# Kernel optimization log

Hardware: AMD Instinct MI355X
Metric: run time of the kernel (lower is better)

## Reference

```python
import jax, jax.numpy as jnp
import numpy as np

B, N, L, D = 128, 1024, 512, 64


def setup_inputs() -> dict:
    key = jax.random.key(0)
    k1, k2 = jax.random.split(key)
    text_outputs = jax.random.normal(k1, (B, N, D), dtype=jnp.float32)
    image_outputs = jax.random.normal(k2, (B, L, D), dtype=jnp.float32)
    rng = np.random.RandomState(0)
    ntok = rng.randint(N // 4, N + 1, size=B)
    nreg = rng.randint(L // 4, L + 1, size=B)
    text_mask = (np.arange(N)[None, :] < ntok[:, None]).astype(np.float32)
    image_mask = (np.arange(L)[None, :] < nreg[:, None]).astype(np.float32)
    # impostor indices (torch code samples these with np.random inside forward;
    # here they are fixed constants for determinism), guaranteed != own index
    I_imp = rng.randint(0, B, size=B)
    S_imp = rng.randint(0, B, size=B)
    ar = np.arange(B)
    I_imp = np.where(I_imp == ar, (I_imp + 1) % B, I_imp).astype(np.int32)
    S_imp = np.where(S_imp == ar, (S_imp + 1) % B, S_imp).astype(np.int32)
    return {
        "text_outputs": text_outputs,
        "image_outputs": image_outputs,
        "text_mask": jnp.asarray(text_mask),
        "image_mask": jnp.asarray(image_mask),
        "I_imp_idx": jnp.asarray(I_imp),
        "S_imp_idx": jnp.asarray(S_imp),
    }


def _mean_max_sim(T, I, tmask, imask):
    # T: (N, D) tokens, I: (L, D) regions; masks select the ragged valid prefix.
    M = jnp.einsum('nd,ld->nl', T, I)                       # matchmap (N, L)
    neg = jnp.finfo(M.dtype).min
    mx = jnp.max(jnp.where(imask[None, :] > 0, M, neg), axis=1)  # max over regions
    return jnp.sum(mx * tmask) / jnp.sum(tmask)             # mean over valid tokens


def reference(text_outputs, image_outputs, text_mask, image_mask, I_imp_idx, S_imp_idx, margin=1.0):
    sim = jax.vmap(_mean_max_sim)
    anchor = sim(text_outputs, image_outputs, text_mask, image_mask)            # (B,)
    Simpsim = sim(text_outputs[S_imp_idx], image_outputs, text_mask[S_imp_idx], image_mask)
    Iimpsim = sim(text_outputs, image_outputs[I_imp_idx], text_mask, image_mask[I_imp_idx])
    # scalar per-sample hinge: term added only when margin+imp-anchor > 0 == relu
    per_sample = jax.nn.relu(margin + Iimpsim - anchor) + jax.nn.relu(margin + Simpsim - anchor)
    loss = jnp.sum(per_sample) / text_outputs.shape[0]
    return loss[None]  # torch returns shape (1,)
```

## Files before the change

### kernel.cpp

```cpp
#include <hip/hip_runtime.h>
#include <hip/hip_bf16.h>

#define B 128
#define N 1024
#define L 512
#define D 64

typedef float f32x4 __attribute__((ext_vector_type(4)));
typedef short bf16x8 __attribute__((ext_vector_type(8)));

__device__ inline bf16x8 cvt8(float4 f0, float4 f1) {
    union { __hip_bfloat162 h2[4]; bf16x8 v; } u;
    u.h2[0] = __float22bfloat162_rn(make_float2(f0.x, f0.y));
    u.h2[1] = __float22bfloat162_rn(make_float2(f0.z, f0.w));
    u.h2[2] = __float22bfloat162_rn(make_float2(f1.x, f1.y));
    u.h2[3] = __float22bfloat162_rn(make_float2(f1.z, f1.w));
    return u.v;
}

#define WS_NEED_PRE (8192 + (size_t)B * L * D * 2)

__global__ __launch_bounds__(64) void cnts_kernel(
        const float* __restrict__ tmask, const float* __restrict__ imask,
        int* __restrict__ cnts) {
    int row = blockIdx.x;
    int lane = threadIdx.x;
    float s = 0.f;
    if (row < B) {
        const float* p = tmask + (size_t)row * N;
        for (int i = lane; i < N; i += 64) s += p[i];
    } else {
        const float* p = imask + (size_t)(row - B) * L;
        for (int i = lane; i < L; i += 64) s += p[i];
    }
    for (int off = 32; off > 0; off >>= 1) s += __shfl_down(s, off);
    if (lane == 0) cnts[row] = (int)(s + 0.5f);
}

__global__ __launch_bounds__(256) void prep_kernel(
        const float* __restrict__ I, unsigned short* __restrict__ Ibf) {
    int blk = blockIdx.x;
    int tid = threadIdx.x;
    const float* src = I + (size_t)blk * 64 * D;
    unsigned short* dst = Ibf + (size_t)blk * 4096;
#pragma unroll
    for (int j = 0; j < 2; ++j) {
        int si = tid + j * 256;
        int r = si >> 3, seg = si & 7;
        const float4* p = (const float4*)(src + (size_t)si * 8);
        bf16x8 v = cvt8(p[0], p[1]);
        int h = seg >> 2, qq = seg & 3;
        int ci = ((r >> 4) * 2 + h) * 64 + qq * 16 + (r & 15);
        *(bf16x8*)(dst + (size_t)ci * 8) = v;
    }
}

template <bool PRE>
__global__ __launch_bounds__(256, 6) void sim_kernel(
        const float* __restrict__ T, const float* __restrict__ I,
        const unsigned short* __restrict__ Ibf, const int* __restrict__ cnts,
        const int* __restrict__ Iimp, const int* __restrict__ Simp,
        float* __restrict__ partials) {
    int blk = blockIdx.x;
    int chunk = blk & 3;
    int bs = blk >> 2;
    int b = bs & (B - 1);
    int s = bs >> 7;
    int Tb = b, Ib = b;
    if (s == 1) Tb = Simp[b];
    else if (s == 2) Ib = Iimp[b];
    int ntok = cnts[Tb];
    int nreg = cnts[B + Ib];

    int tid = threadIdx.x;
    int tok0 = chunk * 256;
    if (tok0 >= ntok) {
        if (tid == 0) partials[blk] = 0.f;
        return;
    }

    int w = tid >> 6;
    int lane = tid & 63;
    int q = lane >> 4;
    int c = lane & 15;

    __shared__ unsigned short ldsI[2][64 * D];
    __shared__ float wsum[4];

    int wt0 = tok0 + w * 64;
    bf16x8 afrag[4][2];
#pragma unroll
    for (int tt = 0; tt < 4; ++tt) {
        const float* trow = T + ((size_t)Tb * N + wt0 + tt * 16 + c) * D;
#pragma unroll
        for (int h = 0; h < 2; ++h) {
            const float4* p = (const float4*)(trow + h * 32 + q * 8);
            afrag[tt][h] = cvt8(p[0], p[1]);
        }
    }

    float mx[4][4];
#pragma unroll
    for (int tt = 0; tt < 4; ++tt)
#pragma unroll
        for (int i = 0; i < 4; ++i) mx[tt][i] = -3.0e38f;

    int r_loc[2], db_loc[2];
#pragma unroll
    for (int j = 0; j < 2; ++j) {
        int ci = tid + j * 256;
        int g = ci >> 6, ln = ci & 63;
        r_loc[j] = (g >> 1) * 16 + (ln & 15);
        db_loc[j] = (g & 1) * 32 + (ln >> 4) * 8;
    }

    int nchunks = (nreg + 63) >> 6;
    const char* img = (const char*)(Ibf + (size_t)Ib * 8 * 4096);
    const float* Ibase = I + (size_t)Ib * L * D;
    uint4 pb0, pb1;
    float4 pf[4];

    auto issue = [&](int k) {
        if (PRE) {
            const char* srcb = img + (size_t)k * 8192;
            pb0 = *(const uint4*)(srcb + (size_t)tid * 16);
            pb1 = *(const uint4*)(srcb + (size_t)(tid + 256) * 16);
        } else {
            int rbase = k * 64;
#pragma unroll
            for (int j = 0; j < 2; ++j) {
                int r = rbase + r_loc[j];
                if (r < nreg) {
                    const float4* p = (const float4*)(Ibase + (size_t)r * D + db_loc[j]);
                    pf[2 * j] = p[0];
                    pf[2 * j + 1] = p[1];
                } else {
                    pf[2 * j] = make_float4(0.f, 0.f, 0.f, 0.f);
                    pf[2 * j + 1] = make_float4(0.f, 0.f, 0.f, 0.f);
                }
            }
        }
    };
    auto store = [&](int k) {
        char* bufb = (char*)&ldsI[k & 1][0];
        if (PRE) {
            *(uint4*)(bufb + (size_t)tid * 16) = pb0;
            *(uint4*)(bufb + (size_t)(tid + 256) * 16) = pb1;
        } else {
#pragma unroll
            for (int j = 0; j < 2; ++j) {
                int ci = tid + j * 256;
                *(bf16x8*)(bufb + (size_t)ci * 16) = cvt8(pf[2 * j], pf[2 * j + 1]);
            }
        }
    };

    issue(0);
    store(0);
    __syncthreads();

    for (int k = 0; k < nchunks; ++k) {
        if (k + 1 < nchunks) issue(k + 1);

        const char* base = (const char*)&ldsI[k & 1][0] + (size_t)lane * 16;
        int nvalid = nreg - k * 64;
        if (nvalid > 64) nvalid = 64;
        int nft = nvalid >> 4, prem = nvalid & 15;
        for (int rt = 0; rt < nft; ++rt) {
            bf16x8 b0 = *(const bf16x8*)(base + (size_t)(rt * 2 + 0) * 1024);
            bf16x8 b1 = *(const bf16x8*)(base + (size_t)(rt * 2 + 1) * 1024);
#pragma unroll
            for (int tt = 0; tt < 4; ++tt) {
                f32x4 acc = {0.f, 0.f, 0.f, 0.f};
                acc = __builtin_amdgcn_mfma_f32_16x16x32_bf16(afrag[tt][0], b0, acc, 0, 0, 0);
                acc = __builtin_amdgcn_mfma_f32_16x16x32_bf16(afrag[tt][1], b1, acc, 0, 0, 0);
#pragma unroll
                for (int i = 0; i < 4; ++i) mx[tt][i] = fmaxf(mx[tt][i], acc[i]);
            }
        }
        if (prem) {
            bf16x8 b0 = *(const bf16x8*)(base + (size_t)(nft * 2 + 0) * 1024);
            bf16x8 b1 = *(const bf16x8*)(base + (size_t)(nft * 2 + 1) * 1024);
            bool valid = c < prem;
#pragma unroll
            for (int tt = 0; tt < 4; ++tt) {
                f32x4 acc = {0.f, 0.f, 0.f, 0.f};
                acc = __builtin_amdgcn_mfma_f32_16x16x32_bf16(afrag[tt][0], b0, acc, 0, 0, 0);
                acc = __builtin_amdgcn_mfma_f32_16x16x32_bf16(afrag[tt][1], b1, acc, 0, 0, 0);
                if (valid) {
#pragma unroll
                    for (int i = 0; i < 4; ++i) mx[tt][i] = fmaxf(mx[tt][i], acc[i]);
                }
            }
        }

        if (k + 1 < nchunks) {
            store(k + 1);
            __syncthreads();
        }
    }

#pragma unroll
    for (int m = 1; m < 16; m <<= 1) {
#pragma unroll
        for (int tt = 0; tt < 4; ++tt)
#pragma unroll
            for (int i = 0; i < 4; ++i)
                mx[tt][i] = fmaxf(mx[tt][i], __shfl_xor(mx[tt][i], m));
    }

    float bsum = 0.f;
    if (c == 0) {
#pragma unroll
        for (int tt = 0; tt < 4; ++tt)
#pragma unroll
            for (int i = 0; i < 4; ++i) {
                int row = wt0 + tt * 16 + q * 4 + i;
                if (row < ntok) bsum += mx[tt][i];
            }
    }
    for (int off = 32; off > 0; off >>= 1) bsum += __shfl_down(bsum, off);
    if (lane == 0) wsum[w] = bsum;
    __syncthreads();
    if (tid == 0)
        partials[blk] = (wsum[0] + wsum[1] + wsum[2] + wsum[3]) / (float)ntok;
}

__global__ void loss_kernel(const float* __restrict__ partials,
                            float* __restrict__ out) {
    int tid = threadIdx.x;
    __shared__ float simsL[384];
    __shared__ float w6[6];
    const float4* p4 = (const float4*)partials;
    float4 v = p4[tid];
    simsL[tid] = v.x + v.y + v.z + v.w;
    __syncthreads();
    float per = 0.f;
    if (tid < B) {
        float anc  = simsL[tid];
        float simp = simsL[B + tid];
        float iimp = simsL[2 * B + tid];
        per = fmaxf(1.f + iimp - anc, 0.f) + fmaxf(1.f + simp - anc, 0.f);
    }
    for (int off = 32; off > 0; off >>= 1) per += __shfl_down(per, off);
    if ((tid & 63) == 0) w6[tid >> 6] = per;
    __syncthreads();
    if (tid == 0)
        out[0] = (w6[0] + w6[1] + w6[2] + w6[3] + w6[4] + w6[5]) / (float)B;
}

extern "C" void kernel_launch(void* const* d_in, const int* in_sizes, int n_in,
                              void* d_out, int out_size, void* d_ws, size_t ws_size,
                              hipStream_t stream) {
    const float* T     = (const float*)d_in[0];
    const float* I     = (const float*)d_in[1];
    const float* tmask = (const float*)d_in[2];
    const float* imask = (const float*)d_in[3];
    const int*   Iimp  = (const int*)d_in[4];
    const int*   Simp  = (const int*)d_in[5];

    float* partials = (float*)d_ws;
    int*   cnts     = (int*)((char*)d_ws + 6144);
    unsigned short* Ibf = (unsigned short*)((char*)d_ws + 8192);

    cnts_kernel<<<2 * B, 64, 0, stream>>>(tmask, imask, cnts);
    if (ws_size >= WS_NEED_PRE) {
        prep_kernel<<<B * 8, 256, 0, stream>>>(I, Ibf);
        sim_kernel<true><<<3 * B * 4, 256, 0, stream>>>(T, I, Ibf, cnts, Iimp, Simp, partials);
    } else {
        sim_kernel<false><<<3 * B * 4, 256, 0, stream>>>(T, I, Ibf, cnts, Iimp, Simp, partials);
    }
    loss_kernel<<<1, 384, 0, stream>>>(partials, (float*)d_out);
}
```

Measured before the change: 129.4 us.

## Read pre-converted bf16 image tiles directly from global memory, skipping LDS staging

In the precomputed-bf16 path, each wave now loads its MFMA B fragments straight from the fragment-ordered global buffer, with register double-buffering one row tile ahead. This drops the LDS store, reload and block barriers per 64-region chunk. Each of the four waves now issues the same global loads independently, so L2/L1 traffic goes up. The launch-bounds occupancy hint is also lowered from 6 to 4 blocks to leave more registers per thread.

```diff
diff --git a/kernel.cpp b/kernel.cpp
--- a/kernel.cpp
+++ b/kernel.cpp
@@ -56,7 +56,7 @@
 }
 
 template <bool PRE>
-__global__ __launch_bounds__(256, 6) void sim_kernel(
+__global__ __launch_bounds__(256, 4) void sim_kernel(
         const float* __restrict__ T, const float* __restrict__ I,
         const unsigned short* __restrict__ Ibf, const int* __restrict__ cnts,
         const int* __restrict__ Iimp, const int* __restrict__ Simp,
@@ -84,7 +84,6 @@
     int q = lane >> 4;
     int c = lane & 15;
 
-    __shared__ unsigned short ldsI[2][64 * D];
     __shared__ float wsum[4];
 
     int wt0 = tok0 + w * 64;
@@ -105,27 +104,48 @@
 #pragma unroll
         for (int i = 0; i < 4; ++i) mx[tt][i] = -3.0e38f;
 
-    int r_loc[2], db_loc[2];
-#pragma unroll
-    for (int j = 0; j < 2; ++j) {
-        int ci = tid + j * 256;
-        int g = ci >> 6, ln = ci & 63;
-        r_loc[j] = (g >> 1) * 16 + (ln & 15);
-        db_loc[j] = (g & 1) * 32 + (ln >> 4) * 8;
-    }
-
-    int nchunks = (nreg + 63) >> 6;
-    const char* img = (const char*)(Ibf + (size_t)Ib * 8 * 4096);
-    const float* Ibase = I + (size_t)Ib * L * D;
-    uint4 pb0, pb1;
-    float4 pf[4];
-
-    auto issue = [&](int k) {
-        if (PRE) {
-            const char* srcb = img + (size_t)k * 8192;
-            pb0 = *(const uint4*)(srcb + (size_t)tid * 16);
-            pb1 = *(const uint4*)(srcb + (size_t)(tid + 256) * 16);
-        } else {
+    int nrt = (nreg + 15) >> 4;
+    int prem = nreg & 15;
+
+    if (PRE) {
+        const char* imgL = (const char*)(Ibf + (size_t)Ib * L * D) + (size_t)lane * 16;
+        bf16x8 cb0 = *(const bf16x8*)(imgL);
+        bf16x8 cb1 = *(const bf16x8*)(imgL + 1024);
+#pragma unroll 2
+        for (int rt = 0; rt < nrt; ++rt) {
+            bf16x8 nb0 = cb0, nb1 = cb1;
+            if (rt + 1 < nrt) {
+                const char* p = imgL + (size_t)(rt + 1) * 2048;
+                nb0 = *(const bf16x8*)(p);
+                nb1 = *(const bf16x8*)(p + 1024);
+            }
+            bool vld = (rt + 1 < nrt) || (prem == 0) || (c < prem);
+#pragma unroll
+            for (int tt = 0; tt < 4; ++tt) {
+                f32x4 acc = {0.f, 0.f, 0.f, 0.f};
+                acc = __builtin_amdgcn_mfma_f32_16x16x32_bf16(afrag[tt][0], cb0, acc, 0, 0, 0);
+                acc = __builtin_amdgcn_mfma_f32_16x16x32_bf16(afrag[tt][1], cb1, acc, 0, 0, 0);
+                if (vld) {
+#pragma unroll
+                    for (int i = 0; i < 4; ++i) mx[tt][i] = fmaxf(mx[tt][i], acc[i]);
+                }
+            }
+            cb0 = nb0; cb1 = nb1;
+        }
+    } else {
+        __shared__ unsigned short ldsI[2][64 * D];
+        int r_loc[2], db_loc[2];
+#pragma unroll
+        for (int j = 0; j < 2; ++j) {
+            int ci = tid + j * 256;
+            int g = ci >> 6, ln = ci & 63;
+            r_loc[j] = (g >> 1) * 16 + (ln & 15);
+            db_loc[j] = (g & 1) * 32 + (ln >> 4) * 8;
+        }
+        int nchunks = (nreg + 63) >> 6;
+        const float* Ibase = I + (size_t)Ib * L * D;
+        float4 pf[4];
+        auto issue = [&](int k) {
             int rbase = k * 64;
 #pragma unroll
             for (int j = 0; j < 2; ++j) {
@@ -139,64 +159,50 @@
                     pf[2 * j + 1] = make_float4(0.f, 0.f, 0.f, 0.f);
                 }
             }
-        }
-    };
-    auto store = [&](int k) {
-        char* bufb = (char*)&ldsI[k & 1][0];
-        if (PRE) {
-            *(uint4*)(bufb + (size_t)tid * 16) = pb0;
-            *(uint4*)(bufb + (size_t)(tid + 256) * 16) = pb1;
-        } else {
+        };
+        auto store = [&](int k) {
+            char* bufb = (char*)&ldsI[k & 1][0];
 #pragma unroll
             for (int j = 0; j < 2; ++j) {
                 int ci = tid + j * 256;
                 *(bf16x8*)(bufb + (size_t)ci * 16) = cvt8(pf[2 * j], pf[2 * j + 1]);
             }
-        }
-    };
-
-    issue(0);
-    store(0);
-    __syncthreads();
-
-    for (int k = 0; k < nchunks; ++k) {
-        if (k + 1 < nchunks) issue(k + 1);
-
-        const char* base = (const char*)&ldsI[k & 1][0] + (size_t)lane * 16;
-        int nvalid = nreg - k * 64;
-        if (nvalid > 64) nvalid = 64;
-        int nft = nvalid >> 4, prem = nvalid & 15;
-        for (int rt = 0; rt < nft; ++rt) {
-            bf16x8 b0 = *(const bf16x8*)(base + (size_t)(rt * 2 + 0) * 1024);
-            bf16x8 b1 = *(const bf16x8*)(base + (size_t)(rt * 2 + 1) * 1024);
-#pragma unroll
-            for (int tt = 0; tt < 4; ++tt) {
-                f32x4 acc = {0.f, 0.f, 0.f, 0.f};
-                acc = __builtin_amdgcn_mfma_f32_16x16x32_bf16(afrag[tt][0], b0, acc, 0, 0, 0);
-                acc = __builtin_amdgcn_mfma_f32_16x16x32_bf16(afrag[tt][1], b1, acc, 0, 0, 0);
-#pragma unroll
-                for (int i = 0; i < 4; ++i) mx[tt][i] = fmaxf(mx[tt][i], acc[i]);
-            }
-        }
-        if (prem) {
-            bf16x8 b0 = *(const bf16x8*)(base + (size_t)(nft * 2 + 0) * 1024);
-            bf16x8 b1 = *(const bf16x8*)(base + (size_t)(nft * 2 + 1) * 1024);
-            bool valid = c < prem;
-#pragma unroll
-            for (int tt = 0; tt < 4; ++tt) {
-                f32x4 acc = {0.f, 0.f, 0.f, 0.f};
-                acc = __builtin_amdgcn_mfma_f32_16x16x32_bf16(afrag[tt][0], b0, acc, 0, 0, 0);
-                acc = __builtin_amdgcn_mfma_f32_16x16x32_bf16(afrag[tt][1], b1, acc, 0, 0, 0);
-                if (valid) {
+        };
+        issue(0); store(0); __syncthreads();
+        for (int k = 0; k < nchunks; ++k) {
+            if (k + 1 < nchunks) issue(k + 1);
+            const char* base = (const char*)&ldsI[k & 1][0] + (size_t)lane * 16;
+            int nvalid = nreg - k * 64;
+            if (nvalid > 64) nvalid = 64;
+            int nft = nvalid >> 4, prem2 = nvalid & 15;
+            for (int rt = 0; rt < nft; ++rt) {
+                bf16x8 b0 = *(const bf16x8*)(base + (size_t)(rt * 2 + 0) * 1024);
+                bf16x8 b1 = *(const bf16x8*)(base + (size_t)(rt * 2 + 1) * 1024);
+#pragma unroll
+                for (int tt = 0; tt < 4; ++tt) {
+                    f32x4 acc = {0.f, 0.f, 0.f, 0.f};
+                    acc = __builtin_amdgcn_mfma_f32_16x16x32_bf16(afrag[tt][0], b0, acc, 0, 0, 0);
+                    acc = __builtin_amdgcn_mfma_f32_16x16x32_bf16(afrag[tt][1], b1, acc, 0, 0, 0);
 #pragma unroll
                     for (int i = 0; i < 4; ++i) mx[tt][i] = fmaxf(mx[tt][i], acc[i]);
                 }
             }
-        }
-
-        if (k + 1 < nchunks) {
-            store(k + 1);
-            __syncthreads();
+            if (prem2) {
+                bf16x8 b0 = *(const bf16x8*)(base + (size_t)(nft * 2 + 0) * 1024);
+                bf16x8 b1 = *(const bf16x8*)(base + (size_t)(nft * 2 + 1) * 1024);
+                bool valid = c < prem2;
+#pragma unroll
+                for (int tt = 0; tt < 4; ++tt) {
+                    f32x4 acc = {0.f, 0.f, 0.f, 0.f};
+                    acc = __builtin_amdgcn_mfma_f32_16x16x32_bf16(afrag[tt][0], b0, acc, 0, 0, 0);
+                    acc = __builtin_amdgcn_mfma_f32_16x16x32_bf16(afrag[tt][1], b1, acc, 0, 0, 0);
+                    if (valid) {
+#pragma unroll
+                        for (int i = 0; i < 4; ++i) mx[tt][i] = fmaxf(mx[tt][i], acc[i]);
+                    }
+                }
+            }
+            if (k + 1 < nchunks) { store(k + 1); __syncthreads(); }
         }
     }
 
```

Result: slower. 132.5 us (+2.4%).
